# Performance work log

Measured on AMD Instinct MI355X. Metric: run time of the kernel, lower is better.

Reference implementation:

```python
import jax, jax.numpy as jnp
import numpy as np

GAMMA = 1.0
BIG = 1e8  # boundary sentinel, matches 100000000.0 in the original


def _softdtw_R(D, gamma=GAMMA):
    """Forward soft-DTW DP. D: [N, M] distance matrix -> R: [N, M].
    R[i,j] = D[i,j] + softmin_gamma(R[i-1,j-1], R[i-1,j], R[i,j-1])."""
    N, M = D.shape
    dt = D.dtype

    def row_step(prev_row, d_row):
        # prev_row: [M+1] = padded previous row R[i-1, 0..M] (index 0 = left boundary)
        diag = prev_row[:-1]  # R[i-1, j-1]
        up = prev_row[1:]     # R[i-1, j]

        def cell(r_left, xs):
            dg, u, d = xs
            z = jnp.stack([dg, u, r_left]) * (-1.0 / gamma)
            m = jnp.max(z)
            softmin = -gamma * (jnp.log(jnp.sum(jnp.exp(z - m))) + m)
            r = d + softmin
            return r, r

        _, row = jax.lax.scan(cell, jnp.asarray(BIG, dt), (diag, up, d_row))
        new_prev = jnp.concatenate([jnp.full((1,), BIG, dt), row])
        return new_prev, row

    # padded row 0: corner R[0,0]=0, top boundary = BIG
    init = jnp.concatenate([jnp.zeros((1,), dt), jnp.full((M,), BIG, dt)])
    _, R = jax.lax.scan(row_step, init, D)
    return R  # [N, M]


def reference(x):
    # x: [B, N, M, 1] batch of distance matrices
    D = jnp.squeeze(x, axis=-1)
    R = jax.vmap(_softdtw_R)(D)
    return R[..., None]  # [B, N, M, 1]


def setup_inputs() -> dict:
    key = jax.random.key(0)
    B, N, M = 32, 512, 512
    x = jax.random.uniform(key, (B, N, M, 1), dtype=jnp.float32)
    return {"x": x}
```

## Files before the change

kernel.cpp:

```cpp
#include <hip/hip_runtime.h>

#define N_DIM 512
#define M_DIM 512
#define NQUAD 128
#define TSTEPS 192
#define SLOT4 4096
#define DDEPTH 6
#define RING6 (DDEPTH * SLOT4)
#define SIGMA_MAX (TSTEPS + DDEPTH)
#define BSTRIDE (N_DIM * M_DIM)
#define GSTRIDE (NQUAD * 64)
#define DSKEW_B ((size_t)SIGMA_MAX * SLOT4)
#define ESKEW_B ((size_t)TSTEPS * SLOT4)
#define LN2F 0.6931471805599453f
#define DEPTH 4
#define SLOT_BYTES 8192
#define RING_BYTES (DEPTH * SLOT_BYTES)
#define ROW_BYTES 2048
#define ROW_MAX (511 * 2048)

#define AS1 __attribute__((address_space(1)))
#define AS3 __attribute__((address_space(3)))

__device__ inline unsigned pkbf16(float lo, float hi) {
    unsigned r; asm("v_cvt_pk_bf16_f32 %0, %1, %2" : "=v"(r) : "v"(lo), "v"(hi)); return r;
}
__device__ inline float ubf_lo(unsigned u) { return __int_as_float((int)(u << 16)); }
__device__ inline float ubf_hi(unsigned u) { return __int_as_float((int)(u & 0xffff0000u)); }

__global__ __launch_bounds__(256) void skew_pre(const float* __restrict__ D,
                                                char* __restrict__ Dsk) {
    const int b  = blockIdx.y;
    const int t0 = blockIdx.x << 3;
    __shared__ float4 tile[4096];
    const int tid = threadIdx.x;

    const float4* src = (const float4*)(D + (size_t)b * BSTRIDE) + ((size_t)t0 << 9);
    #pragma unroll
    for (int w = 0; w < 16; ++w) {
        const int idx = (w << 8) + tid;
        const float4 v = src[idx];
        tile[idx] = make_float4(__expf(-v.x), __expf(-v.y), __expf(-v.z), __expf(-v.w));
    }
    __syncthreads();

    char* dst = Dsk + (size_t)b * DSKEW_B;
    #pragma unroll
    for (int w = 0; w < 9; ++w) {
        const int w2 = (w << 8) + tid;
        const int li = w2 & 7;
        const int ch = (w2 >> 3) & 3;
        const int si = w2 >> 5;
        const int lmin = max(0, si - 7);
        const int l = lmin + li;
        if (si < 71 && l <= min(63, si)) {
            const int ti = si - l;
            const int base = (((ti << 2) + ch) << 7) + (l << 1);
            const float4 a = tile[base];
            const float4 c = tile[base + 1];
            uint4 o;
            o.x = pkbf16(a.x, a.y); o.y = pkbf16(a.z, a.w);
            o.z = pkbf16(c.x, c.y); o.w = pkbf16(c.z, c.w);
            *(uint4*)(dst + (size_t)(t0 + si) * SLOT4 + (ch << 10) + (l << 4)) = o;
        }
    }
}

__global__ __launch_bounds__(256) void unskew_post(const char* __restrict__ Esk,
                                                   const float* __restrict__ gm,
                                                   float* __restrict__ R) {
    const int b  = blockIdx.y;
    const int t0 = blockIdx.x << 3;
    __shared__ float4 tile[4096];
    const int tid = threadIdx.x;

    const char* srcE = Esk + (size_t)b * ESKEW_B;
    #pragma unroll
    for (int w = 0; w < 9; ++w) {
        const int w2 = (w << 8) + tid;
        const int li = w2 & 7;
        const int ch = (w2 >> 3) & 3;
        const int si = w2 >> 5;
        const int lmin = max(0, si - 7);
        const int l = lmin + li;
        if (si < 71 && l <= min(63, si)) {
            const int ti = si - l;
            const uint4 v = *(const uint4*)(srcE + (size_t)(t0 + si) * SLOT4
                                            + (ch << 10) + (l << 4));
            const int base = (((ti << 2) + ch) << 7) + (l << 1);
            tile[base]     = make_float4(ubf_lo(v.x), ubf_hi(v.x), ubf_lo(v.y), ubf_hi(v.y));
            tile[base + 1] = make_float4(ubf_lo(v.z), ubf_hi(v.z), ubf_lo(v.w), ubf_hi(v.w));
        }
    }
    __syncthreads();

    float* dstR = R + (size_t)b * BSTRIDE;
    const float* gmb = gm + b * GSTRIDE;
    #pragma unroll
    for (int w = 0; w < 16; ++w) {
        const int idx = (w << 8) + tid;
        const int rit = idx >> 7;
        const int c4  = idx & 127;
        const int tq  = t0 + (rit >> 2);
        const float g = gmb[(tq << 6) + (c4 >> 1)];
        const float4 v = tile[idx];
        *(float4*)(dstR + (((size_t)(t0 << 2) + rit) << 9) + (c4 << 2)) =
            make_float4(g - __logf(v.x), g - __logf(v.y), g - __logf(v.z), g - __logf(v.w));
    }
}

__global__ __launch_bounds__(256) void log_post_plain(float4* __restrict__ E4,
                                                      const float* __restrict__ gm, int n4) {
    int i = blockIdx.x * blockDim.x + threadIdx.x;
    const int stride = gridDim.x * blockDim.x;
    for (; i < n4; i += stride) {
        const int b   = i >> 16;
        const int rem = i & 65535;
        const int row = rem >> 7;
        const int c4  = rem & 127;
        const float g = gm[(b << 13) + ((row >> 2) << 6) + (c4 >> 1)];
        const float4 v = E4[i];
        E4[i] = make_float4(g - __logf(v.x), g - __logf(v.y),
                            g - __logf(v.z), g - __logf(v.w));
    }
}

__device__ inline float shup1(float x) {
    int r = __builtin_amdgcn_update_dpp(0, __float_as_int(x), 0x138, 0xf, 0xf, true);
    return __int_as_float(r);
}
__device__ inline int shup1i(int x) {
    return __builtin_amdgcn_update_dpp(0, x, 0x138, 0xf, 0xf, true);
}
__device__ inline int fr_exp(float x) {
    int e; asm("v_frexp_exp_i32_f32 %0, %1" : "=v"(e) : "v"(x)); return e;
}
__device__ inline float ldx(float x, int k) {
    float r; asm("v_ldexp_f32 %0, %1, %2" : "=v"(r) : "v"(x), "v"(k)); return r;
}

__global__ __launch_bounds__(64, 1) void softdtw_dp_skew(const char* __restrict__ Dsk,
                                                         char* __restrict__ Esk,
                                                         float* __restrict__ gmap) {
    const int b = blockIdx.x;
    const int l = threadIdx.x;
    const int laneB16 = l << 4;

    const char* __restrict__ DskB = Dsk + (size_t)b * DSKEW_B;
    char*       __restrict__ EskB = Esk + (size_t)b * ESKEW_B;
    float*      __restrict__ gm   = gmap + (size_t)b * GSTRIDE;

    __shared__ char ring[RING6] __attribute__((aligned(16)));
    const unsigned ring_base = (unsigned)(size_t)(AS3 char*)ring;

    float Ep[8];
    #pragma unroll
    for (int k = 0; k < 8; ++k) Ep[k] = 0.0f;
    float fQ = 0.0f;
    int   KG = 0, KE = 0, Kh = 0;
    float expA7 = 0.0f, expB7 = 0.0f, expC7 = 0.0f, expD7 = 0.0f;
    float E7hD = 0.0f;

    int dsk_off = DDEPTH * SLOT4;
    int es_off  = 0;
    unsigned dma_wo = 0;
    unsigned rd_wo  = SLOT4;

    uint4 P[4], Nx[4];
    #pragma unroll
    for (int ch = 0; ch < 4; ++ch)
        P[ch] = *(const uint4*)(DskB + ch * 1024 + laneB16);
    #pragma unroll
    for (int sig = 1; sig < DDEPTH; ++sig) {
        const char* gp = DskB + sig * SLOT4 + laneB16;
        #pragma unroll
        for (int ch = 0; ch < 4; ++ch)
            __builtin_amdgcn_global_load_lds((const AS1 void*)(gp + ch * 1024),
                                             (AS3 void*)(ring + sig * SLOT4 + ch * 1024),
                                             16, 0, 0);
    }
    asm volatile("s_waitcnt vmcnt(0)" ::: "memory");

    auto step = [&](int s, uint4 (&cur)[4], uint4 (&nxt)[4]) {
        {
            const char* gp = DskB + dsk_off + laneB16;
            #pragma unroll
            for (int ch = 0; ch < 4; ++ch)
                __builtin_amdgcn_global_load_lds((const AS1 void*)(gp + ch * 1024),
                                                 (AS3 void*)(ring + dma_wo + ch * 1024), 16, 0, 0);
            dsk_off += SLOT4;
        }
        asm volatile("s_waitcnt vmcnt(45)" ::: "memory");

        const float E7sA = shup1(expA7);
        const float E7sB = shup1(expB7);
        const float E7sC = shup1(expC7);
        const float E7sD = shup1(expD7);
        const int   Ks   = shup1i(KE);

        const unsigned raddr = ring_base + rd_wo + (unsigned)laneB16;
        asm volatile("ds_read_b128 %0, %4 offset:0\n\t"
                     "ds_read_b128 %1, %4 offset:1024\n\t"
                     "ds_read_b128 %2, %4 offset:2048\n\t"
                     "ds_read_b128 %3, %4 offset:3072"
                     : "=&v"(nxt[0]), "=&v"(nxt[1]), "=&v"(nxt[2]), "=&v"(nxt[3])
                     : "v"(raddr));

        asm volatile("s_waitcnt lgkmcnt(4)" ::: "memory");
        __builtin_amdgcn_sched_barrier(0);

        const int t = s - l;
        if (t >= 0 && t < NQUAD) {
            float end_[4][8];
            #pragma unroll
            for (int r = 0; r < 4; ++r) {
                end_[r][0] = ubf_lo(cur[r].x); end_[r][1] = ubf_hi(cur[r].x);
                end_[r][2] = ubf_lo(cur[r].y); end_[r][3] = ubf_hi(cur[r].y);
                end_[r][4] = ubf_lo(cur[r].z); end_[r][5] = ubf_hi(cur[r].z);
                end_[r][6] = ubf_lo(cur[r].w); end_[r][7] = ubf_hi(cur[r].w);
            }

            const bool is0    = (t == 0);
            const bool origin = is0 && (l == 0);
            int K = is0 ? (Ks - fr_exp(E7sA)) : KG;
            K = origin ? 0 : K;
            const float fq = is0 ? 0.0f : fQ;
            const int dKs = K - Ks;
            const int dKh = K - Kh;

            float eL[4];
            eL[0] = ldx(E7sA, dKs);
            eL[1] = ldx(E7sB, dKs);
            eL[2] = ldx(E7sC, dKs);
            eL[3] = ldx(E7sD, dKs);
            float eD0 = ldx(E7hD, dKh);
            eD0 = is0 ? 0.0f : eD0;
            eD0 = origin ? 1.0f : eD0;

            float Fp[8];
            #pragma unroll
            for (int c = 0; c < 8; ++c) Fp[c] = fq * Ep[c];

            float Ev[4][8];
            #pragma unroll
            for (int d = 0; d <= 10; ++d) {
                #pragma unroll
                for (int r = 0; r < 4; ++r) {
                    const int c = d - r;
                    if (c >= 0 && c < 8) {
                        float q;
                        if (r == 0) q = (c == 0) ? (eD0 + Fp[0]) : (Fp[c - 1] + Fp[c]);
                        else        q = (c == 0) ? (eL[r - 1] + Ev[r - 1][0])
                                                 : (Ev[r - 1][c - 1] + Ev[r - 1][c]);
                        const float ein = (c == 0) ? eL[r] : Ev[r][c - 1];
                        Ev[r][c] = __builtin_fmaf(end_[r][c], ein, end_[r][c] * q);
                    }
                }
            }

            char* sb = EskB + es_off + laneB16;
            #pragma unroll
            for (int r = 0; r < 4; ++r) {
                uint4 o;
                o.x = pkbf16(Ev[r][0], Ev[r][1]); o.y = pkbf16(Ev[r][2], Ev[r][3]);
                o.z = pkbf16(Ev[r][4], Ev[r][5]); o.w = pkbf16(Ev[r][6], Ev[r][7]);
                *(uint4*)(sb + r * 1024) = o;
            }
            gm[(t << 6) + l] = (float)K * LN2F;

            const int ed = fr_exp(Ev[3][0]);
            KG = K - ed;
            fQ = ldx(1.0f, -ed);
            KE = K;
            #pragma unroll
            for (int c = 0; c < 8; ++c) Ep[c] = Ev[3][c];
            expA7 = Ev[0][7]; expB7 = Ev[1][7]; expC7 = Ev[2][7]; expD7 = Ev[3][7];
        }

        E7hD = E7sD;
        Kh   = Ks;
        es_off += SLOT4;
        dma_wo = (dma_wo == (DDEPTH - 1) * SLOT4) ? 0u : dma_wo + SLOT4;
        rd_wo  = (rd_wo  == (DDEPTH - 1) * SLOT4) ? 0u : rd_wo  + SLOT4;
    };

    for (int s = 0; s < TSTEPS; s += 2) {
        step(s,     P,  Nx);
        step(s + 1, Nx, P);
    }
}

__global__ __launch_bounds__(64, 1) void softdtw_dp_direct(const float* __restrict__ Dsrc,
                                                           float* __restrict__ Eout,
                                                           float* __restrict__ gmap) {
    const int b     = blockIdx.x;
    const int l     = threadIdx.x;
    const int laneB = l << 5;
    const float* __restrict__ Db = Dsrc + (size_t)b * BSTRIDE;
    float*       __restrict__ Rb = Eout + (size_t)b * BSTRIDE;
    float*       __restrict__ gm = gmap + (size_t)b * GSTRIDE;
    __shared__ char ring[RING_BYTES] __attribute__((aligned(16)));
    const unsigned ring_base = (unsigned)(size_t)(AS3 char*)ring;

    float Ep[8];
    #pragma unroll
    for (int k = 0; k < 8; ++k) Ep[k] = 0.0f;
    float fQ = 0.0f;
    int KG = 0, KE = 0, Kh = 0;
    float expA7 = 0.0f, expB7 = 0.0f, expC7 = 0.0f, expD7 = 0.0f;
    float E7hD = 0.0f;
    int raw[4];
    #pragma unroll
    for (int k = 0; k < 4; ++k) raw[k] = (16 + k) * ROW_BYTES - (l << 13);
    int soff = -(l << 13);

    float4 P[8], Nx[8];
    #pragma unroll
    for (int row = 0; row < 4; ++row) {
        const int r = min(max(-4 * l + row, 0), N_DIM - 1);
        P[2 * row]     = *(const float4*)(Db + (size_t)r * M_DIM + (l << 3));
        P[2 * row + 1] = *(const float4*)(Db + (size_t)r * M_DIM + (l << 3) + 4);
    }
    #pragma unroll
    for (int sig = 1; sig < DEPTH; ++sig) {
        const unsigned wo = (unsigned)sig * SLOT_BYTES;
        #pragma unroll
        for (int k = 0; k < 4; ++k) {
            const int cl = min(max((4 * (sig - l) + k) * ROW_BYTES, 0), ROW_MAX);
            const char* gp = (const char*)Db + cl + laneB;
            __builtin_amdgcn_global_load_lds((const AS1 void*)gp,
                                             (AS3 void*)(ring + wo + (2 * k) * 1024), 16, 0, 0);
            __builtin_amdgcn_global_load_lds((const AS1 void*)(gp + 16),
                                             (AS3 void*)(ring + wo + (2 * k + 1) * 1024), 16, 0, 0);
        }
    }
    asm volatile("s_waitcnt vmcnt(0)" ::: "memory");

    auto rowfma = [&](const float* endv, float eLeft, const float* Q, float* E) {
        float e = eLeft;
        #pragma unroll
        for (int c = 0; c < 8; ++c) {
            e = __builtin_fmaf(endv[c], e, endv[c] * Q[c]);
            E[c] = e;
        }
    };

    auto step = [&](int s, float4 (&cur)[8], float4 (&nxt)[8]) {
        {
            const unsigned wo = ((unsigned)(s + DEPTH) & (DEPTH - 1)) * SLOT_BYTES;
            #pragma unroll
            for (int k = 0; k < 4; ++k) {
                const int cl = min(max(raw[k], 0), ROW_MAX);
                const char* gp = (const char*)Db + cl + laneB;
                __builtin_amdgcn_global_load_lds((const AS1 void*)gp,
                                                 (AS3 void*)(ring + wo + (2 * k) * 1024), 16, 0, 0);
                __builtin_amdgcn_global_load_lds((const AS1 void*)(gp + 16),
                                                 (AS3 void*)(ring + wo + (2 * k + 1) * 1024), 16, 0, 0);
                raw[k] += 4 * ROW_BYTES;
            }
        }
        asm volatile("s_waitcnt vmcnt(51)" ::: "memory");
        const float E7sA = shup1(expA7);
        const float E7sB = shup1(expB7);
        const float E7sC = shup1(expC7);
        const float E7sD = shup1(expD7);
        const int   Ks   = shup1i(KE);
        const unsigned raddr = ring_base
                             + (unsigned)((s + 1) & (DEPTH - 1)) * SLOT_BYTES
                             + (unsigned)l * 16u;
        asm volatile("ds_read_b128 %0, %8 offset:0\n\t"
                     "ds_read_b128 %1, %8 offset:1024\n\t"
                     "ds_read_b128 %2, %8 offset:2048\n\t"
                     "ds_read_b128 %3, %8 offset:3072\n\t"
                     "ds_read_b128 %4, %8 offset:4096\n\t"
                     "ds_read_b128 %5, %8 offset:5120\n\t"
                     "ds_read_b128 %6, %8 offset:6144\n\t"
                     "ds_read_b128 %7, %8 offset:7168"
                     : "=&v"(nxt[0]), "=&v"(nxt[1]), "=&v"(nxt[2]), "=&v"(nxt[3]),
                       "=&v"(nxt[4]), "=&v"(nxt[5]), "=&v"(nxt[6]), "=&v"(nxt[7])
                     : "v"(raddr));
        asm volatile("s_waitcnt lgkmcnt(8)" ::: "memory");
        __builtin_amdgcn_sched_barrier(0);
        const int t = s - l;
        if (t >= 0 && t < NQUAD) {
            const float endA[8] = {__expf(-cur[0].x), __expf(-cur[0].y), __expf(-cur[0].z), __expf(-cur[0].w),
                                   __expf(-cur[1].x), __expf(-cur[1].y), __expf(-cur[1].z), __expf(-cur[1].w)};
            const float endB[8] = {__expf(-cur[2].x), __expf(-cur[2].y), __expf(-cur[2].z), __expf(-cur[2].w),
                                   __expf(-cur[3].x), __expf(-cur[3].y), __expf(-cur[3].z), __expf(-cur[3].w)};
            const float endC[8] = {__expf(-cur[4].x), __expf(-cur[4].y), __expf(-cur[4].z), __expf(-cur[4].w),
                                   __expf(-cur[5].x), __expf(-cur[5].y), __expf(-cur[5].z), __expf(-cur[5].w)};
            const float endD[8] = {__expf(-cur[6].x), __expf(-cur[6].y), __expf(-cur[6].z), __expf(-cur[6].w),
                                   __expf(-cur[7].x), __expf(-cur[7].y), __expf(-cur[7].z), __expf(-cur[7].w)};
            const bool is0    = (t == 0);
            const bool origin = is0 && (l == 0);
            int K = is0 ? (Ks - fr_exp(E7sA)) : KG;
            K = origin ? 0 : K;
            const float fq = is0 ? 0.0f : fQ;
            const int dKs = K - Ks;
            const int dKh = K - Kh;
            const float eLA = ldx(E7sA, dKs);
            const float eLB = ldx(E7sB, dKs);
            const float eLC = ldx(E7sC, dKs);
            const float eLD = ldx(E7sD, dKs);
            float eDA0 = ldx(E7hD, dKh);
            eDA0 = is0 ? 0.0f : eDA0;
            eDA0 = origin ? 1.0f : eDA0;
            float QA[8];
            QA[0] = eDA0 + fq * Ep[0];
            #pragma unroll
            for (int c = 1; c < 8; ++c) QA[c] = fq * (Ep[c - 1] + Ep[c]);
            float EA[8]; rowfma(endA, eLA, QA, EA);
            float QB[8];
            QB[0] = eLA + EA[0];
            #pragma unroll
            for (int c = 1; c < 8; ++c) QB[c] = EA[c - 1] + EA[c];
            float EB[8]; rowfma(endB, eLB, QB, EB);
            float QC[8];
            QC[0] = eLB + EB[0];
            #pragma unroll
            for (int c = 1; c < 8; ++c) QC[c] = EB[c - 1] + EB[c];
            float EC[8]; rowfma(endC, eLC, QC, EC);
            float QD[8];
            QD[0] = eLC + EC[0];
            #pragma unroll
            for (int c = 1; c < 8; ++c) QD[c] = EC[c - 1] + EC[c];
            float ED[8]; rowfma(endD, eLD, QD, ED);
            char* sb  = (char*)Rb + soff + laneB;
            char* sb2 = sb + 4096;
            *(float4*)(sb)         = make_float4(EA[0], EA[1], EA[2], EA[3]);
            *(float4*)(sb + 16)    = make_float4(EA[4], EA[5], EA[6], EA[7]);
            *(float4*)(sb + 2048)  = make_float4(EB[0], EB[1], EB[2], EB[3]);
            *(float4*)(sb + 2064)  = make_float4(EB[4], EB[5], EB[6], EB[7]);
            *(float4*)(sb2)        = make_float4(EC[0], EC[1], EC[2], EC[3]);
            *(float4*)(sb2 + 16)   = make_float4(EC[4], EC[5], EC[6], EC[7]);
            *(float4*)(sb2 + 2048) = make_float4(ED[0], ED[1], ED[2], ED[3]);
            *(float4*)(sb2 + 2064) = make_float4(ED[4], ED[5], ED[6], ED[7]);
            gm[(t << 6) + l] = (float)K * LN2F;
            const int ed = fr_exp(ED[0]);
            KG = K - ed;
            fQ = ldx(1.0f, -ed);
            KE = K;
            #pragma unroll
            for (int c = 0; c < 8; ++c) Ep[c] = ED[c];
            expA7 = EA[7]; expB7 = EB[7]; expC7 = EC[7]; expD7 = ED[7];
        }
        E7hD = E7sD;
        Kh   = Ks;
        soff += 4 * ROW_BYTES;
    };

    for (int s = 0; s < TSTEPS; s += 2) {
        step(s,     P,  Nx);
        step(s + 1, Nx, P);
    }
}

extern "C" void kernel_launch(void* const* d_in, const int* in_sizes, int n_in,
                              void* d_out, int out_size, void* d_ws, size_t ws_size,
                              hipStream_t stream) {
    const float* x = (const float*)d_in[0];
    float* out     = (float*)d_out;
    const int B    = in_sizes[0] / BSTRIDE;
    const size_t GMAP_BYTES = (size_t)B * GSTRIDE * sizeof(float);
    const size_t need_skew  = (size_t)B * (DSKEW_B + ESKEW_B) + GMAP_BYTES;

    if (ws_size >= need_skew) {
        char*  dsk = (char*)d_ws;
        char*  esk = dsk + (size_t)B * DSKEW_B;
        float* gm  = (float*)(esk + (size_t)B * ESKEW_B);
        skew_pre<<<dim3(16, B), dim3(256), 0, stream>>>(x, dsk);
        softdtw_dp_skew<<<dim3(B), dim3(64), 0, stream>>>(dsk, esk, gm);
        unskew_post<<<dim3(16, B), dim3(256), 0, stream>>>(esk, gm, out);
    } else {
        float* gm = (float*)d_ws;
        const int n4 = (B * BSTRIDE) / 4;
        softdtw_dp_direct<<<dim3(B), dim3(64), 0, stream>>>(x, out, gm);
        log_post_plain<<<dim3(2048), dim3(256), 0, stream>>>((float4*)out, gm, n4);
    }
}
```

Before: 117.0 us.

## Process two batch elements per wavefront in skewed soft-DTW DP kernel

The DP kernel now runs two independent batch problems interleaved in one 64-lane wavefront, so the wavefront gets two independent dependency chains for instruction-level parallelism. The grid is halved to B/2 blocks. The LDS ring depth drops from 6 to 4 slots per problem, with power-of-two modulo indexing in place of the compare-and-wrap counters. The trade-off is fewer concurrent wavefronts across the GPU (16 instead of 32), higher register pressure, and a shallower prefetch depth.

```diff
diff --git a/kernel.cpp b/kernel.cpp
--- a/kernel.cpp
+++ b/kernel.cpp
@@ -5,8 +5,8 @@
 #define NQUAD 128
 #define TSTEPS 192
 #define SLOT4 4096
-#define DDEPTH 6
-#define RING6 (DDEPTH * SLOT4)
+#define DDEPTH 4
+#define RINGP (DDEPTH * SLOT4)
 #define SIGMA_MAX (TSTEPS + DDEPTH)
 #define BSTRIDE (N_DIM * M_DIM)
 #define GSTRIDE (NQUAD * 64)
@@ -139,149 +139,174 @@
     float r; asm("v_ldexp_f32 %0, %1, %2" : "=v"(r) : "v"(x), "v"(k)); return r;
 }
 
-__global__ __launch_bounds__(64, 1) void softdtw_dp_skew(const char* __restrict__ Dsk,
-                                                         char* __restrict__ Esk,
-                                                         float* __restrict__ gmap) {
-    const int b = blockIdx.x;
-    const int l = threadIdx.x;
+__global__ __launch_bounds__(64, 1) void softdtw_dp_skew2(const char* __restrict__ Dsk,
+                                                          char* __restrict__ Esk,
+                                                          float* __restrict__ gmap) {
+    const int bp = blockIdx.x;
+    const int l  = threadIdx.x;
     const int laneB16 = l << 4;
 
-    const char* __restrict__ DskB = Dsk + (size_t)b * DSKEW_B;
-    char*       __restrict__ EskB = Esk + (size_t)b * ESKEW_B;
-    float*      __restrict__ gm   = gmap + (size_t)b * GSTRIDE;
-
-    __shared__ char ring[RING6] __attribute__((aligned(16)));
-    const unsigned ring_base = (unsigned)(size_t)(AS3 char*)ring;
-
-    float Ep[8];
-    #pragma unroll
-    for (int k = 0; k < 8; ++k) Ep[k] = 0.0f;
-    float fQ = 0.0f;
-    int   KG = 0, KE = 0, Kh = 0;
-    float expA7 = 0.0f, expB7 = 0.0f, expC7 = 0.0f, expD7 = 0.0f;
-    float E7hD = 0.0f;
+    const char* DskB[2] = { Dsk + (size_t)(2 * bp)     * DSKEW_B,
+                            Dsk + (size_t)(2 * bp + 1) * DSKEW_B };
+    char*       EskB[2] = { Esk + (size_t)(2 * bp)     * ESKEW_B,
+                            Esk + (size_t)(2 * bp + 1) * ESKEW_B };
+    float*      gmB[2]  = { gmap + (size_t)(2 * bp)     * GSTRIDE,
+                            gmap + (size_t)(2 * bp + 1) * GSTRIDE };
+
+    __shared__ char ring[2 * RINGP] __attribute__((aligned(16)));
+    const unsigned rbase[2] = { (unsigned)(size_t)(AS3 char*)ring,
+                                (unsigned)(size_t)(AS3 char*)ring + RINGP };
+
+    float Ep[2][8];
+    float fQ[2] = {0.0f, 0.0f};
+    int   KG[2] = {0, 0}, KE[2] = {0, 0}, Kh[2] = {0, 0};
+    float ex0[2] = {0,0}, ex1[2] = {0,0}, ex2[2] = {0,0}, ex3[2] = {0,0};
+    float E7hD[2] = {0, 0};
+    #pragma unroll
+    for (int p = 0; p < 2; ++p)
+        #pragma unroll
+        for (int k = 0; k < 8; ++k) Ep[p][k] = 0.0f;
 
     int dsk_off = DDEPTH * SLOT4;
     int es_off  = 0;
-    unsigned dma_wo = 0;
-    unsigned rd_wo  = SLOT4;
-
-    uint4 P[4], Nx[4];
-    #pragma unroll
-    for (int ch = 0; ch < 4; ++ch)
-        P[ch] = *(const uint4*)(DskB + ch * 1024 + laneB16);
-    #pragma unroll
-    for (int sig = 1; sig < DDEPTH; ++sig) {
-        const char* gp = DskB + sig * SLOT4 + laneB16;
+
+    uint4 P[2][4], Nx[2][4];
+    #pragma unroll
+    for (int p = 0; p < 2; ++p)
         #pragma unroll
         for (int ch = 0; ch < 4; ++ch)
-            __builtin_amdgcn_global_load_lds((const AS1 void*)(gp + ch * 1024),
-                                             (AS3 void*)(ring + sig * SLOT4 + ch * 1024),
-                                             16, 0, 0);
-    }
-    asm volatile("s_waitcnt vmcnt(0)" ::: "memory");
-
-    auto step = [&](int s, uint4 (&cur)[4], uint4 (&nxt)[4]) {
-        {
-            const char* gp = DskB + dsk_off + laneB16;
+            P[p][ch] = *(const uint4*)(DskB[p] + ch * 1024 + laneB16);
+    #pragma unroll
+    for (int sig = 1; sig < DDEPTH; ++sig)
+        #pragma unroll
+        for (int p = 0; p < 2; ++p) {
+            const char* gp = DskB[p] + sig * SLOT4 + laneB16;
             #pragma unroll
             for (int ch = 0; ch < 4; ++ch)
                 __builtin_amdgcn_global_load_lds((const AS1 void*)(gp + ch * 1024),
-                                                 (AS3 void*)(ring + dma_wo + ch * 1024), 16, 0, 0);
+                                                 (AS3 void*)(ring + p * RINGP + sig * SLOT4 + ch * 1024),
+                                                 16, 0, 0);
+        }
+    asm volatile("s_waitcnt vmcnt(0)" ::: "memory");
+
+    auto step = [&](int s, uint4 (&cur)[2][4], uint4 (&nxt)[2][4]) {
+        {
+            const unsigned wo = ((unsigned)s & (DDEPTH - 1)) * SLOT4;
+            #pragma unroll
+            for (int p = 0; p < 2; ++p) {
+                const char* gp = DskB[p] + dsk_off + laneB16;
+                #pragma unroll
+                for (int ch = 0; ch < 4; ++ch)
+                    __builtin_amdgcn_global_load_lds((const AS1 void*)(gp + ch * 1024),
+                                                     (AS3 void*)(ring + p * RINGP + wo + ch * 1024),
+                                                     16, 0, 0);
+            }
             dsk_off += SLOT4;
         }
-        asm volatile("s_waitcnt vmcnt(45)" ::: "memory");
-
-        const float E7sA = shup1(expA7);
-        const float E7sB = shup1(expB7);
-        const float E7sC = shup1(expC7);
-        const float E7sD = shup1(expD7);
-        const int   Ks   = shup1i(KE);
-
-        const unsigned raddr = ring_base + rd_wo + (unsigned)laneB16;
-        asm volatile("ds_read_b128 %0, %4 offset:0\n\t"
-                     "ds_read_b128 %1, %4 offset:1024\n\t"
-                     "ds_read_b128 %2, %4 offset:2048\n\t"
-                     "ds_read_b128 %3, %4 offset:3072"
-                     : "=&v"(nxt[0]), "=&v"(nxt[1]), "=&v"(nxt[2]), "=&v"(nxt[3])
-                     : "v"(raddr));
-
-        asm volatile("s_waitcnt lgkmcnt(4)" ::: "memory");
+        asm volatile("s_waitcnt vmcnt(54)" ::: "memory");
+
+        float E7sA[2], E7sB[2], E7sC[2], E7sD[2];
+        int Ks[2];
+        #pragma unroll
+        for (int p = 0; p < 2; ++p) {
+            E7sA[p] = shup1(ex0[p]);
+            E7sB[p] = shup1(ex1[p]);
+            E7sC[p] = shup1(ex2[p]);
+            E7sD[p] = shup1(ex3[p]);
+            Ks[p]   = shup1i(KE[p]);
+        }
+
+        const unsigned ro = ((unsigned)(s + 1) & (DDEPTH - 1)) * SLOT4 + (unsigned)laneB16;
+        asm volatile("ds_read_b128 %0, %8 offset:0\n\t"
+                     "ds_read_b128 %1, %8 offset:1024\n\t"
+                     "ds_read_b128 %2, %8 offset:2048\n\t"
+                     "ds_read_b128 %3, %8 offset:3072\n\t"
+                     "ds_read_b128 %4, %9 offset:0\n\t"
+                     "ds_read_b128 %5, %9 offset:1024\n\t"
+                     "ds_read_b128 %6, %9 offset:2048\n\t"
+                     "ds_read_b128 %7, %9 offset:3072"
+                     : "=&v"(nxt[0][0]), "=&v"(nxt[0][1]), "=&v"(nxt[0][2]), "=&v"(nxt[0][3]),
+                       "=&v"(nxt[1][0]), "=&v"(nxt[1][1]), "=&v"(nxt[1][2]), "=&v"(nxt[1][3])
+                     : "v"(rbase[0] + ro), "v"(rbase[1] + ro));
+
+        asm volatile("s_waitcnt lgkmcnt(8)" ::: "memory");
         __builtin_amdgcn_sched_barrier(0);
 
         const int t = s - l;
         if (t >= 0 && t < NQUAD) {
-            float end_[4][8];
-            #pragma unroll
-            for (int r = 0; r < 4; ++r) {
-                end_[r][0] = ubf_lo(cur[r].x); end_[r][1] = ubf_hi(cur[r].x);
-                end_[r][2] = ubf_lo(cur[r].y); end_[r][3] = ubf_hi(cur[r].y);
-                end_[r][4] = ubf_lo(cur[r].z); end_[r][5] = ubf_hi(cur[r].z);
-                end_[r][6] = ubf_lo(cur[r].w); end_[r][7] = ubf_hi(cur[r].w);
-            }
-
-            const bool is0    = (t == 0);
-            const bool origin = is0 && (l == 0);
-            int K = is0 ? (Ks - fr_exp(E7sA)) : KG;
-            K = origin ? 0 : K;
-            const float fq = is0 ? 0.0f : fQ;
-            const int dKs = K - Ks;
-            const int dKh = K - Kh;
-
-            float eL[4];
-            eL[0] = ldx(E7sA, dKs);
-            eL[1] = ldx(E7sB, dKs);
-            eL[2] = ldx(E7sC, dKs);
-            eL[3] = ldx(E7sD, dKs);
-            float eD0 = ldx(E7hD, dKh);
-            eD0 = is0 ? 0.0f : eD0;
-            eD0 = origin ? 1.0f : eD0;
-
-            float Fp[8];
-            #pragma unroll
-            for (int c = 0; c < 8; ++c) Fp[c] = fq * Ep[c];
-
-            float Ev[4][8];
-            #pragma unroll
-            for (int d = 0; d <= 10; ++d) {
+            #pragma unroll
+            for (int p = 0; p < 2; ++p) {
+                float end_[4][8];
                 #pragma unroll
                 for (int r = 0; r < 4; ++r) {
-                    const int c = d - r;
-                    if (c >= 0 && c < 8) {
-                        float q;
-                        if (r == 0) q = (c == 0) ? (eD0 + Fp[0]) : (Fp[c - 1] + Fp[c]);
-                        else        q = (c == 0) ? (eL[r - 1] + Ev[r - 1][0])
-                                                 : (Ev[r - 1][c - 1] + Ev[r - 1][c]);
-                        const float ein = (c == 0) ? eL[r] : Ev[r][c - 1];
-                        Ev[r][c] = __builtin_fmaf(end_[r][c], ein, end_[r][c] * q);
+                    end_[r][0] = ubf_lo(cur[p][r].x); end_[r][1] = ubf_hi(cur[p][r].x);
+                    end_[r][2] = ubf_lo(cur[p][r].y); end_[r][3] = ubf_hi(cur[p][r].y);
+                    end_[r][4] = ubf_lo(cur[p][r].z); end_[r][5] = ubf_hi(cur[p][r].z);
+                    end_[r][6] = ubf_lo(cur[p][r].w); end_[r][7] = ubf_hi(cur[p][r].w);
+                }
+
+                const bool is0    = (t == 0);
+                const bool origin = is0 && (l == 0);
+                int K = is0 ? (Ks[p] - fr_exp(E7sA[p])) : KG[p];
+                K = origin ? 0 : K;
+                const float fq = is0 ? 0.0f : fQ[p];
+                const int dKs = K - Ks[p];
+                const int dKh = K - Kh[p];
+
+                float eL[4];
+                eL[0] = ldx(E7sA[p], dKs);
+                eL[1] = ldx(E7sB[p], dKs);
+                eL[2] = ldx(E7sC[p], dKs);
+                eL[3] = ldx(E7sD[p], dKs);
+                float eD0 = ldx(E7hD[p], dKh);
+                eD0 = is0 ? 0.0f : eD0;
+                eD0 = origin ? 1.0f : eD0;
+
+                float Fp[8];
+                #pragma unroll
+                for (int c = 0; c < 8; ++c) Fp[c] = fq * Ep[p][c];
+
+                float Ev[4][8];
+                #pragma unroll
+                for (int d = 0; d <= 10; ++d) {
+                    #pragma unroll
+                    for (int r = 0; r < 4; ++r) {
+                        const int c = d - r;
+                        if (c >= 0 && c < 8) {
+                            float q;
+                            if (r == 0) q = (c == 0) ? (eD0 + Fp[0]) : (Fp[c - 1] + Fp[c]);
+                            else        q = (c == 0) ? (eL[r - 1] + Ev[r - 1][0])
+                                                     : (Ev[r - 1][c - 1] + Ev[r - 1][c]);
+                            const float ein = (c == 0) ? eL[r] : Ev[r][c - 1];
+                            Ev[r][c] = __builtin_fmaf(end_[r][c], ein, end_[r][c] * q);
+                        }
                     }
                 }
+
+                char* sb = EskB[p] + es_off + laneB16;
+                #pragma unroll
+                for (int r = 0; r < 4; ++r) {
+                    uint4 o;
+                    o.x = pkbf16(Ev[r][0], Ev[r][1]); o.y = pkbf16(Ev[r][2], Ev[r][3]);
+                    o.z = pkbf16(Ev[r][4], Ev[r][5]); o.w = pkbf16(Ev[r][6], Ev[r][7]);
+                    *(uint4*)(sb + r * 1024) = o;
+                }
+                gmB[p][(t << 6) + l] = (float)K * LN2F;
+
+                const int ed = fr_exp(Ev[3][0]);
+                KG[p] = K - ed;
+                fQ[p] = ldx(1.0f, -ed);
+                KE[p] = K;
+                #pragma unroll
+                for (int c = 0; c < 8; ++c) Ep[p][c] = Ev[3][c];
+                ex0[p] = Ev[0][7]; ex1[p] = Ev[1][7];
+                ex2[p] = Ev[2][7]; ex3[p] = Ev[3][7];
             }
-
-            char* sb = EskB + es_off + laneB16;
-            #pragma unroll
-            for (int r = 0; r < 4; ++r) {
-                uint4 o;
-                o.x = pkbf16(Ev[r][0], Ev[r][1]); o.y = pkbf16(Ev[r][2], Ev[r][3]);
-                o.z = pkbf16(Ev[r][4], Ev[r][5]); o.w = pkbf16(Ev[r][6], Ev[r][7]);
-                *(uint4*)(sb + r * 1024) = o;
-            }
-            gm[(t << 6) + l] = (float)K * LN2F;
-
-            const int ed = fr_exp(Ev[3][0]);
-            KG = K - ed;
-            fQ = ldx(1.0f, -ed);
-            KE = K;
-            #pragma unroll
-            for (int c = 0; c < 8; ++c) Ep[c] = Ev[3][c];
-            expA7 = Ev[0][7]; expB7 = Ev[1][7]; expC7 = Ev[2][7]; expD7 = Ev[3][7];
-        }
-
-        E7hD = E7sD;
-        Kh   = Ks;
+        }
+
+        #pragma unroll
+        for (int p = 0; p < 2; ++p) { E7hD[p] = E7sD[p]; Kh[p] = Ks[p]; }
         es_off += SLOT4;
-        dma_wo = (dma_wo == (DDEPTH - 1) * SLOT4) ? 0u : dma_wo + SLOT4;
-        rd_wo  = (rd_wo  == (DDEPTH - 1) * SLOT4) ? 0u : rd_wo  + SLOT4;
     };
 
     for (int s = 0; s < TSTEPS; s += 2) {
@@ -464,12 +489,12 @@
     const size_t GMAP_BYTES = (size_t)B * GSTRIDE * sizeof(float);
     const size_t need_skew  = (size_t)B * (DSKEW_B + ESKEW_B) + GMAP_BYTES;
 
-    if (ws_size >= need_skew) {
+    if (ws_size >= need_skew && (B & 1) == 0) {
         char*  dsk = (char*)d_ws;
         char*  esk = dsk + (size_t)B * DSKEW_B;
         float* gm  = (float*)(esk + (size_t)B * ESKEW_B);
         skew_pre<<<dim3(16, B), dim3(256), 0, stream>>>(x, dsk);
-        softdtw_dp_skew<<<dim3(B), dim3(64), 0, stream>>>(dsk, esk, gm);
+        softdtw_dp_skew2<<<dim3(B / 2), dim3(64), 0, stream>>>(dsk, esk, gm);
         unskew_post<<<dim3(16, B), dim3(256), 0, stream>>>(esk, gm, out);
     } else {
         float* gm = (float*)d_ws;
```

New measurement: 200.3 us. +71.2%, slower.
